# Performance work log

Hardware: AMD Instinct MI355X
Metric: run time of the kernel (lower is better)

Reference implementation:

```python
import jax, jax.numpy as jnp
import numpy as np

NB_FEAT = 20000
NB_CLASSES = 30
N_EDGES = 640000
BATCH = 128


def setup_inputs() -> dict:
    key = jax.random.key(0)
    k1, k2, k3, k4, k5 = jax.random.split(key, 5)
    x = jax.random.normal(k1, (BATCH, NB_FEAT), dtype=jnp.float32)
    edge_index = jax.random.randint(k2, (2, N_EDGES), 0, NB_FEAT, dtype=jnp.int64)
    edge_weight = jax.random.uniform(k3, (N_EDGES,), dtype=jnp.float32)
    fc_w = jax.random.normal(k4, (NB_CLASSES, NB_FEAT), dtype=jnp.float32) * 0.01
    fc_b = jax.random.normal(k5, (NB_CLASSES,), dtype=jnp.float32) * 0.01
    return {"x": x, "edge_index": edge_index, "edge_weight": edge_weight,
            "fc_w": fc_w, "fc_b": fc_b}


def reference(x, edge_index, edge_weight, fc_w, fc_b):
    # SGConv(K=1, bias=False, lin.weight frozen to 1) == gcn_norm + one propagation.
    B, N = x.shape
    src, dst = edge_index[0], edge_index[1]
    # add self-loops with weight 1 (gcn_norm default fill_value=1)
    loop = jnp.arange(N)
    src_f = jnp.concatenate([src, loop])
    dst_f = jnp.concatenate([dst, loop])
    w_f = jnp.concatenate([edge_weight, jnp.ones((N,), edge_weight.dtype)])
    # symmetric normalization: deg over target index
    deg = jax.ops.segment_sum(w_f, dst_f, num_segments=N)  # (N,)
    dinv = jnp.where(deg > 0, jax.lax.rsqrt(deg), 0.0)
    wn = dinv[src_f] * w_f * dinv[dst_f]  # (E',)
    # batched gather-multiply-scatter; graph shared across batch, so vectorize over B
    msgs = x[:, src_f] * wn  # (B, E')
    diffused = jax.ops.segment_sum(msgs.T, dst_f, num_segments=N).T  # (B, N)
    # dropout p=0 -> no-op; dense FC + softmax
    logits = diffused @ fc_w.T + fc_b  # (B, C)
    return jax.nn.softmax(logits, axis=1)
```

## Files before the change

### kernel.cpp

```cpp
#include <hip/hip_runtime.h>


#define N_NODES   20000
#define N_EDGES_C 640000
#define N_CLASSES 30
#define CPAD      32

#define HBLKS     64
#define HNODES    10000
#define HEDGES    (N_EDGES_C / HBLKS)

#define BN        64
#define NBUCKET   313
#define NPB       (NBUCKET * BN)
#define NSLAB     256
#define SLAB_E    (N_EDGES_C / NSLAB)
#define NSCAN     (NBUCKET * NSLAB)
#define ECAP      2600

#define NCHUNK    64
#define NCHUNKS   313
#define XL_LD     130
#define GT_LD     68
#define GBX       128

#define DINVB     ((N_NODES + 255) / 256)

__global__ __launch_bounds__(256) void k1_hists(const int* __restrict__ src,
        const int* __restrict__ dst, const float* __restrict__ w,
        float* __restrict__ degp, int* __restrict__ cnt) {
    __shared__ float h[HNODES];
    int bid = blockIdx.x;
    if (bid < 2 * HBLKS) {
        int eb = bid >> 1, half = bid & 1;
        int nbase = half * HNODES;
        for (int i = threadIdx.x; i < HNODES; i += 256) h[i] = 0.f;
        __syncthreads();
        const int4* d4 = (const int4*)(dst + eb * HEDGES);
        const float4* w4 = (const float4*)(w + eb * HEDGES);
        for (int i = threadIdx.x; i < HEDGES / 4; i += 256) {
            int4 dv = d4[i]; float4 wv = w4[i];
            unsigned r;
            r = (unsigned)(dv.x - nbase); if (r < HNODES) atomicAdd(&h[r], wv.x);
            r = (unsigned)(dv.y - nbase); if (r < HNODES) atomicAdd(&h[r], wv.y);
            r = (unsigned)(dv.z - nbase); if (r < HNODES) atomicAdd(&h[r], wv.z);
            r = (unsigned)(dv.w - nbase); if (r < HNODES) atomicAdd(&h[r], wv.w);
        }
        __syncthreads();
        float* outp = degp + (size_t)bid * HNODES;
        for (int i = threadIdx.x; i < HNODES; i += 256) outp[i] = h[i];
    } else {
        int slab = bid - 2 * HBLKS;
        int* bc = (int*)h;
        for (int i = threadIdx.x; i < NBUCKET; i += 256) bc[i] = 0;
        __syncthreads();
        const int4* s4 = (const int4*)(src + slab * SLAB_E);
        for (int i = threadIdx.x; i < SLAB_E / 4; i += 256) {
            int4 v = s4[i];
            atomicAdd(&bc[v.x >> 6], 1);
            atomicAdd(&bc[v.y >> 6], 1);
            atomicAdd(&bc[v.z >> 6], 1);
            atomicAdd(&bc[v.w >> 6], 1);
        }
        __syncthreads();
        for (int b = threadIdx.x; b < NBUCKET; b += 256) cnt[b * NSLAB + slab] = bc[b];
    }
}

__global__ __launch_bounds__(256) void k2_prep(const int* __restrict__ cnt,
        int* __restrict__ btot, const float* __restrict__ fc_w,
        const float* __restrict__ degp, float* __restrict__ fc_wT,
        float* __restrict__ dinv) {
    int bid = blockIdx.x;
    int t = threadIdx.x;
    if (bid < NBUCKET) {
        __shared__ int lds[256];
        lds[t] = cnt[bid * NSLAB + t];
        __syncthreads();
        for (int o = 128; o > 0; o >>= 1) {
            if (t < o) lds[t] += lds[t + o];
            __syncthreads();
        }
        if (t == 0) btot[bid] = lds[0];
    } else if (bid < 2 * NBUCKET) {
        __shared__ float tile[CPAD][65];
        int n0 = (bid - NBUCKET) * 64;
        #pragma unroll
        for (int k = 0; k < 8; k++) {
            int c = k * 4 + (t >> 6), nn = t & 63;
            int n = n0 + nn;
            tile[c][nn] = (c < N_CLASSES && n < N_NODES) ? fc_w[c * N_NODES + n] : 0.f;
        }
        __syncthreads();
        #pragma unroll
        for (int k = 0; k < 8; k++) {
            int idx = k * 256 + t;
            int nn = idx >> 5, c = idx & 31;
            fc_wT[(size_t)(n0 + nn) * CPAD + c] = tile[c][nn];
        }
    } else {
        int n = (bid - 2 * NBUCKET) * 256 + t;
        if (n < N_NODES) {
            int half = n / HNODES, nn = n - half * HNODES;
            float s = 1.0f;
            for (int eb = 0; eb < HBLKS; eb++)
                s += degp[(size_t)((eb << 1) | half) * HNODES + nn];
            dinv[n] = rsqrtf(s);
        }
    }
}

__global__ __launch_bounds__(256) void k3_off(const int* __restrict__ cnt,
        const int* __restrict__ btot, int* __restrict__ off) {
    __shared__ int lds[256];
    __shared__ int bb;
    int b = blockIdx.x, t = threadIdx.x;
    int s = 0;
    for (int i = t; i < b; i += 256) s += btot[i];
    lds[t] = s;
    __syncthreads();
    for (int o = 128; o > 0; o >>= 1) {
        if (t < o) lds[t] += lds[t + o];
        __syncthreads();
    }
    if (t == 0) bb = lds[0];
    __syncthreads();
    int base = bb;
    int v = cnt[b * NSLAB + t];
    lds[t] = v;
    __syncthreads();
    for (int o = 1; o < 256; o <<= 1) {
        int u = (t >= o) ? lds[t - o] : 0;
        __syncthreads();
        lds[t] += u;
        __syncthreads();
    }
    off[b * NSLAB + t] = base + lds[t] - v;
    if (b == NBUCKET - 1 && t == 255) off[NSCAN] = base + lds[t];
}

__global__ __launch_bounds__(512) void k4_scatter(const int* __restrict__ src,
        const int* __restrict__ dst, const float* __restrict__ w,
        const float* __restrict__ dinv, const int* __restrict__ off,
        int2* __restrict__ erec) {
    __shared__ int cur[NBUCKET];
    int slab = blockIdx.x;
    for (int b = threadIdx.x; b < NBUCKET; b += 512) cur[b] = off[b * NSLAB + slab];
    __syncthreads();
    int e0 = slab * SLAB_E;
    const int4* s4 = (const int4*)(src + e0);
    const int4* d4 = (const int4*)(dst + e0);
    const float4* w4 = (const float4*)(w + e0);
    for (int i = threadIdx.x; i < SLAB_E / 4; i += 512) {
        int4 sv = s4[i]; int4 dv = d4[i]; float4 wv = w4[i];
        int s, d, p; float wn;
        s = sv.x; d = dv.x; wn = dinv[s] * wv.x * dinv[d];
        p = atomicAdd(&cur[s >> 6], 1);
        erec[p] = make_int2(((s & 63) << 15) | d, __float_as_int(wn));
        s = sv.y; d = dv.y; wn = dinv[s] * wv.y * dinv[d];
        p = atomicAdd(&cur[s >> 6], 1);
        erec[p] = make_int2(((s & 63) << 15) | d, __float_as_int(wn));
        s = sv.z; d = dv.z; wn = dinv[s] * wv.z * dinv[d];
        p = atomicAdd(&cur[s >> 6], 1);
        erec[p] = make_int2(((s & 63) << 15) | d, __float_as_int(wn));
        s = sv.w; d = dv.w; wn = dinv[s] * wv.w * dinv[d];
        p = atomicAdd(&cur[s >> 6], 1);
        erec[p] = make_int2(((s & 63) << 15) | d, __float_as_int(wn));
    }
}

__global__ __launch_bounds__(512) void k5_fold(const int2* __restrict__ erec,
        const int* __restrict__ off, const float* __restrict__ dinv,
        const float* __restrict__ fc_wT, float* __restrict__ gT) {
    __shared__ int2 srt[ECAP];
    __shared__ int hist[BN];
    __shared__ int rowst[BN];
    __shared__ int cur[BN];
    int bucket = blockIdx.x;
    int nlo = bucket * BN;
    int bstart = off[bucket * NSLAB];
    int bend   = off[(bucket + 1) * NSLAB];
    int len = min(bend - bstart, ECAP);
    if (threadIdx.x < BN) hist[threadIdx.x] = 0;
    __syncthreads();
    for (int i = threadIdx.x; i < len; i += 512)
        atomicAdd(&hist[((unsigned)erec[bstart + i].x) >> 15], 1);
    __syncthreads();
    if (threadIdx.x < BN) {
        int h = hist[threadIdx.x];
        int v = h;
        #pragma unroll
        for (int o = 1; o < BN; o <<= 1) {
            int u = __shfl_up(v, o, 64);
            if (threadIdx.x >= o) v += u;
        }
        rowst[threadIdx.x] = v - h;
        cur[threadIdx.x]   = v - h;
    }
    __syncthreads();
    for (int i = threadIdx.x; i < len; i += 512) {
        int2 r = erec[bstart + i];
        int p = atomicAdd(&cur[((unsigned)r.x) >> 15], 1);
        srt[p] = r;
    }
    __syncthreads();
    int c = threadIdx.x & 31;
    int grp = threadIdx.x >> 5;
    for (int nn = grp; nn < BN; nn += 16) {
        int n = nlo + nn;
        if (n >= N_NODES) {
            if (n < NPB) gT[(size_t)n * CPAD + c] = 0.f;
            continue;
        }
        float di = dinv[n];
        float acc  = di * di * fc_wT[(size_t)n * CPAD + c];
        float acc2 = 0.f;
        int i = rowst[nn], re = i + hist[nn];
        for (; i + 1 < re; i += 2) {
            int2 r0 = srt[i], r1 = srt[i + 1];
            acc  += __int_as_float(r0.y) * fc_wT[(size_t)(r0.x & 0x7FFF) * CPAD + c];
            acc2 += __int_as_float(r1.y) * fc_wT[(size_t)(r1.x & 0x7FFF) * CPAD + c];
        }
        if (i < re) {
            int2 r0 = srt[i];
            acc += __int_as_float(r0.y) * fc_wT[(size_t)(r0.x & 0x7FFF) * CPAD + c];
        }
        gT[(size_t)n * CPAD + c] = acc + acc2;
    }
}

__global__ __launch_bounds__(512) void k6_gemm(const float* __restrict__ x,
        const float* __restrict__ gT, float* __restrict__ part) {
    __shared__ float xl[(NCHUNK / 2) * XL_LD];
    __shared__ float gt[CPAD * GT_LD];
    int bx = blockIdx.x, bh = blockIdx.y;
    int b0 = bh * 64;
    int wv = threadIdx.x >> 6, l = threadIdx.x & 63;
    float acc0 = 0.f, acc1 = 0.f, acc2 = 0.f, acc3 = 0.f;
    for (int j = 0; j < 3; j++) {
        int ch = bx + GBX * j;
        if (ch >= NCHUNKS) break;
        int n0 = ch * NCHUNK;
        for (int o = threadIdx.x; o < 64 * NCHUNK; o += 512) {
            int b = o >> 6, n = o & (NCHUNK - 1);
            int gn = n0 + n;
            float v = (gn < N_NODES) ? x[(size_t)(b0 + b) * N_NODES + gn] : 0.f;
            xl[(n >> 1) * XL_LD + b * 2 + (n & 1)] = v;
        }
        for (int o = threadIdx.x; o < NCHUNK * CPAD; o += 512) {
            int n = o >> 5, cc = o & 31;
            gt[cc * GT_LD + n] = gT[(size_t)n0 * CPAD + o];
        }
        __syncthreads();
        #pragma unroll
        for (int n4 = 0; n4 < NCHUNK / 4; n4++) {
            float2 xa = *(const float2*)&xl[(2 * n4) * XL_LD + l * 2];
            float2 xb = *(const float2*)&xl[(2 * n4 + 1) * XL_LD + l * 2];
            float4 ga = *(const float4*)&gt[(wv)      * GT_LD + 4 * n4];
            float4 gb = *(const float4*)&gt[(wv +  8) * GT_LD + 4 * n4];
            float4 gc = *(const float4*)&gt[(wv + 16) * GT_LD + 4 * n4];
            float4 gd = *(const float4*)&gt[(wv + 24) * GT_LD + 4 * n4];
            acc0 += xa.x * ga.x + xa.y * ga.y + xb.x * ga.z + xb.y * ga.w;
            acc1 += xa.x * gb.x + xa.y * gb.y + xb.x * gb.z + xb.y * gb.w;
            acc2 += xa.x * gc.x + xa.y * gc.y + xb.x * gc.z + xb.y * gc.w;
            acc3 += xa.x * gd.x + xa.y * gd.y + xb.x * gd.z + xb.y * gd.w;
        }
        __syncthreads();
    }
    size_t pb = (size_t)(bx * 2 + bh) * CPAD * 64;
    part[pb + (size_t)(wv)      * 64 + l] = acc0;
    part[pb + (size_t)(wv +  8) * 64 + l] = acc1;
    part[pb + (size_t)(wv + 16) * 64 + l] = acc2;
    part[pb + (size_t)(wv + 24) * 64 + l] = acc3;
}

__global__ __launch_bounds__(1024) void k7_final(const float* __restrict__ part,
        const float* __restrict__ fc_b, float* __restrict__ out) {
    __shared__ float lg[64 * 33];
    int bh = blockIdx.x;
    int l = threadIdx.x & 63;
    int cq = threadIdx.x >> 6;
    float s0 = 0.f, s1 = 0.f;
    for (int bx = 0; bx < GBX; bx++) {
        const float* p = part + (size_t)(bx * 2 + bh) * CPAD * 64;
        s0 += p[cq * 64 + l];
        s1 += p[(cq + 16) * 64 + l];
    }
    lg[l * 33 + cq]      = s0 + ((cq < N_CLASSES) ? fc_b[cq] : 0.f);
    lg[l * 33 + cq + 16] = s1 + ((cq + 16 < N_CLASSES) ? fc_b[cq + 16] : 0.f);
    __syncthreads();
    if (threadIdx.x < 64) {
        int b = bh * 64 + threadIdx.x;
        float v[N_CLASSES], m = -1e30f;
        #pragma unroll
        for (int c = 0; c < N_CLASSES; c++) {
            v[c] = lg[threadIdx.x * 33 + c];
            m = fmaxf(m, v[c]);
        }
        float s = 0.f;
        #pragma unroll
        for (int c = 0; c < N_CLASSES; c++) { v[c] = __expf(v[c] - m); s += v[c]; }
        float inv = 1.0f / s;
        #pragma unroll
        for (int c = 0; c < N_CLASSES; c++) out[b * N_CLASSES + c] = v[c] * inv;
    }
}

extern "C" void kernel_launch(void* const* d_in, const int* in_sizes, int n_in,
                              void* d_out, int out_size, void* d_ws, size_t ws_size,
                              hipStream_t stream) {
    const float* x          = (const float*)d_in[0];
    const int*   edge_index = (const int*)d_in[1];
    const float* ew         = (const float*)d_in[2];
    const float* fc_w       = (const float*)d_in[3];
    const float* fc_b       = (const float*)d_in[4];
    float* out = (float*)d_out;

    const int* src = edge_index;
    const int* dst = edge_index + N_EDGES_C;

    float* A     = (float*)d_ws;
    float* B     = A + 1280000;
    float* dinv  = B + 1280000;
    int*   cnt   = (int*)(dinv + N_NODES);
    int*   off   = cnt + NSCAN;
    int*   btot  = off + 80136;
    float* fc_wT = (float*)(btot + 320);
    float* gT    = fc_wT + (size_t)NPB * CPAD;

    k1_hists<<<2 * HBLKS + NSLAB, 256, 0, stream>>>(src, dst, ew, A, cnt);
    k2_prep<<<2 * NBUCKET + DINVB, 256, 0, stream>>>(cnt, btot, fc_w, A,
                                                     fc_wT, dinv);
    k3_off<<<NBUCKET, 256, 0, stream>>>(cnt, btot, off);
    k4_scatter<<<NSLAB, 512, 0, stream>>>(src, dst, ew, dinv, off, (int2*)B);
    k5_fold<<<NBUCKET, 512, 0, stream>>>((int2*)B, off, dinv, fc_wT, gT);
    k6_gemm<<<dim3(GBX, 2), 512, 0, stream>>>(x, gT, A);
    k7_final<<<2, 1024, 0, stream>>>(A, fc_b, out);
}
```

Measured before the change: 92.33 us.

## Fuse seven pipeline kernels into one cooperative persistent kernel with grid syncs

Replaces the seven separate kernel launches with a single cooperative kernel of 256 blocks that runs every stage in sequence, separated by grid-wide barriers, and keeps the multi-kernel path as a fallback if the cooperative launch fails. The aim is to remove per-launch overhead and the inter-kernel gaps in a short pipeline. It also halves the number of degree-histogram edge blocks and uses 512 threads per block throughout. In exchange, each stage is limited to 256 resident blocks, the grid syncs add their own cost, and the shared-memory union raises per-block LDS use.

Result: slower. 296.5 us (+221.1%).

```diff
diff --git a/kernel.cpp b/kernel.cpp
--- a/kernel.cpp
+++ b/kernel.cpp
@@ -1,4 +1,7 @@
 #include <hip/hip_runtime.h>
+#include <hip/hip_cooperative_groups.h>
+
+namespace cg = cooperative_groups;
 
 
 #define N_NODES   20000
@@ -6,7 +9,7 @@
 #define N_CLASSES 30
 #define CPAD      32
 
-#define HBLKS     64
+#define HBLKS     32
 #define HNODES    10000
 #define HEDGES    (N_EDGES_C / HBLKS)
 
@@ -24,7 +27,296 @@
 #define GT_LD     68
 #define GBX       128
 
+#define GRID      256
+#define TPB       512
 #define DINVB     ((N_NODES + 255) / 256)
+
+union SMem {
+    float hist[HNODES];
+    int   bc[NBUCKET];
+    int   cur[NBUCKET];
+    float tile[CPAD][65];
+    struct { int lds[TPB]; int bb; } scan;
+    struct { int2 srt[ECAP]; int hist[BN]; int rowst[BN]; int cur[BN]; } fold;
+    struct { float xl[(NCHUNK / 2) * XL_LD]; float gt[CPAD * GT_LD]; } gemm;
+    float lg[64 * 33];
+};
+
+__global__ __launch_bounds__(TPB, 2) void mega(
+        const int* __restrict__ src, const int* __restrict__ dst,
+        const float* __restrict__ ew, const float* __restrict__ x,
+        const float* __restrict__ fc_w, const float* __restrict__ fc_b,
+        float* __restrict__ out,
+        float* __restrict__ degp,
+        int2* __restrict__ erec,
+        float* __restrict__ dinv, int* __restrict__ cnt, int* __restrict__ off,
+        int* __restrict__ btot, float* __restrict__ fc_wT, float* __restrict__ gT) {
+    cg::grid_group grid = cg::this_grid();
+    __shared__ SMem sm;
+    int t = threadIdx.x;
+    float* part = degp;
+
+    for (int u = blockIdx.x; u < 2 * HBLKS + NSLAB + NBUCKET; u += GRID) {
+        if (u < 2 * HBLKS) {
+            int eb = u >> 1, half = u & 1;
+            int nbase = half * HNODES;
+            for (int i = t; i < HNODES; i += TPB) sm.hist[i] = 0.f;
+            __syncthreads();
+            const int4* d4 = (const int4*)(dst + eb * HEDGES);
+            const float4* w4 = (const float4*)(ew + eb * HEDGES);
+            for (int i = t; i < HEDGES / 4; i += TPB) {
+                int4 dv = d4[i]; float4 wv = w4[i];
+                unsigned r;
+                r = (unsigned)(dv.x - nbase); if (r < HNODES) atomicAdd(&sm.hist[r], wv.x);
+                r = (unsigned)(dv.y - nbase); if (r < HNODES) atomicAdd(&sm.hist[r], wv.y);
+                r = (unsigned)(dv.z - nbase); if (r < HNODES) atomicAdd(&sm.hist[r], wv.z);
+                r = (unsigned)(dv.w - nbase); if (r < HNODES) atomicAdd(&sm.hist[r], wv.w);
+            }
+            __syncthreads();
+            float* outp = degp + (size_t)u * HNODES;
+            for (int i = t; i < HNODES; i += TPB) outp[i] = sm.hist[i];
+        } else if (u < 2 * HBLKS + NSLAB) {
+            int slab = u - 2 * HBLKS;
+            for (int i = t; i < NBUCKET; i += TPB) sm.bc[i] = 0;
+            __syncthreads();
+            const int4* s4 = (const int4*)(src + slab * SLAB_E);
+            for (int i = t; i < SLAB_E / 4; i += TPB) {
+                int4 v = s4[i];
+                atomicAdd(&sm.bc[v.x >> 6], 1);
+                atomicAdd(&sm.bc[v.y >> 6], 1);
+                atomicAdd(&sm.bc[v.z >> 6], 1);
+                atomicAdd(&sm.bc[v.w >> 6], 1);
+            }
+            __syncthreads();
+            for (int b = t; b < NBUCKET; b += TPB) cnt[b * NSLAB + slab] = sm.bc[b];
+        } else {
+            int n0 = (u - 2 * HBLKS - NSLAB) * 64;
+            #pragma unroll
+            for (int k = 0; k < 4; k++) {
+                int idx = k * TPB + t; int c = idx >> 6, nn = idx & 63;
+                int n = n0 + nn;
+                sm.tile[c][nn] = (c < N_CLASSES && n < N_NODES) ? fc_w[c * N_NODES + n] : 0.f;
+            }
+            __syncthreads();
+            #pragma unroll
+            for (int k = 0; k < 4; k++) {
+                int idx = k * TPB + t; int nn = idx >> 5, c = idx & 31;
+                fc_wT[(size_t)(n0 + nn) * CPAD + c] = sm.tile[c][nn];
+            }
+        }
+        __syncthreads();
+    }
+    grid.sync();
+
+    for (int u = blockIdx.x; u < NBUCKET + 40; u += GRID) {
+        if (u < NBUCKET) {
+            sm.scan.lds[t] = (t < NSLAB) ? cnt[u * NSLAB + t] : 0;
+            __syncthreads();
+            for (int o = TPB / 2; o > 0; o >>= 1) {
+                if (t < o) sm.scan.lds[t] += sm.scan.lds[t + o];
+                __syncthreads();
+            }
+            if (t == 0) btot[u] = sm.scan.lds[0];
+        } else {
+            int n = (u - NBUCKET) * TPB + t;
+            if (n < N_NODES) {
+                int half = n / HNODES, nn = n - half * HNODES;
+                float s = 1.0f;
+                for (int eb = 0; eb < HBLKS; eb++)
+                    s += degp[(size_t)((eb << 1) | half) * HNODES + nn];
+                dinv[n] = rsqrtf(s);
+            }
+        }
+        __syncthreads();
+    }
+    grid.sync();
+
+    for (int b = blockIdx.x; b < NBUCKET; b += GRID) {
+        int s = 0;
+        for (int i = t; i < b; i += TPB) s += btot[i];
+        sm.scan.lds[t] = s;
+        __syncthreads();
+        for (int o = TPB / 2; o > 0; o >>= 1) {
+            if (t < o) sm.scan.lds[t] += sm.scan.lds[t + o];
+            __syncthreads();
+        }
+        if (t == 0) sm.scan.bb = sm.scan.lds[0];
+        __syncthreads();
+        int base = sm.scan.bb;
+        int v = (t < NSLAB) ? cnt[b * NSLAB + t] : 0;
+        if (t < NSLAB) sm.scan.lds[t] = v;
+        __syncthreads();
+        for (int o = 1; o < NSLAB; o <<= 1) {
+            int u2 = (t < NSLAB && t >= o) ? sm.scan.lds[t - o] : 0;
+            __syncthreads();
+            if (t < NSLAB) sm.scan.lds[t] += u2;
+            __syncthreads();
+        }
+        if (t < NSLAB) off[b * NSLAB + t] = base + sm.scan.lds[t] - v;
+        if (b == NBUCKET - 1 && t == NSLAB - 1) off[NSCAN] = base + sm.scan.lds[t];
+        __syncthreads();
+    }
+    grid.sync();
+
+    for (int slab = blockIdx.x; slab < NSLAB; slab += GRID) {
+        for (int b = t; b < NBUCKET; b += TPB) sm.cur[b] = off[b * NSLAB + slab];
+        __syncthreads();
+        int e0 = slab * SLAB_E;
+        const int4* s4 = (const int4*)(src + e0);
+        const int4* d4 = (const int4*)(dst + e0);
+        const float4* w4 = (const float4*)(ew + e0);
+        for (int i = t; i < SLAB_E / 4; i += TPB) {
+            int4 sv = s4[i]; int4 dv = d4[i]; float4 wv = w4[i];
+            int s, d, p; float wn;
+            s = sv.x; d = dv.x; wn = dinv[s] * wv.x * dinv[d];
+            p = atomicAdd(&sm.cur[s >> 6], 1);
+            erec[p] = make_int2(((s & 63) << 15) | d, __float_as_int(wn));
+            s = sv.y; d = dv.y; wn = dinv[s] * wv.y * dinv[d];
+            p = atomicAdd(&sm.cur[s >> 6], 1);
+            erec[p] = make_int2(((s & 63) << 15) | d, __float_as_int(wn));
+            s = sv.z; d = dv.z; wn = dinv[s] * wv.z * dinv[d];
+            p = atomicAdd(&sm.cur[s >> 6], 1);
+            erec[p] = make_int2(((s & 63) << 15) | d, __float_as_int(wn));
+            s = sv.w; d = dv.w; wn = dinv[s] * wv.w * dinv[d];
+            p = atomicAdd(&sm.cur[s >> 6], 1);
+            erec[p] = make_int2(((s & 63) << 15) | d, __float_as_int(wn));
+        }
+        __syncthreads();
+    }
+    grid.sync();
+
+    for (int bucket = blockIdx.x; bucket < NBUCKET; bucket += GRID) {
+        int nlo = bucket * BN;
+        int bstart = off[bucket * NSLAB];
+        int bend   = off[(bucket + 1) * NSLAB];
+        int len = min(bend - bstart, ECAP);
+        if (t < BN) sm.fold.hist[t] = 0;
+        __syncthreads();
+        for (int i = t; i < len; i += TPB)
+            atomicAdd(&sm.fold.hist[((unsigned)erec[bstart + i].x) >> 15], 1);
+        __syncthreads();
+        if (t < BN) {
+            int h = sm.fold.hist[t];
+            int v = h;
+            #pragma unroll
+            for (int o = 1; o < BN; o <<= 1) {
+                int u2 = __shfl_up(v, o, 64);
+                if (t >= o) v += u2;
+            }
+            sm.fold.rowst[t] = v - h;
+            sm.fold.cur[t]   = v - h;
+        }
+        __syncthreads();
+        for (int i = t; i < len; i += TPB) {
+            int2 r = erec[bstart + i];
+            int p = atomicAdd(&sm.fold.cur[((unsigned)r.x) >> 15], 1);
+            sm.fold.srt[p] = r;
+        }
+        __syncthreads();
+        int c = t & 31;
+        int grp = t >> 5;
+        for (int nn = grp; nn < BN; nn += 16) {
+            int n = nlo + nn;
+            if (n >= N_NODES) {
+                if (n < NPB) gT[(size_t)n * CPAD + c] = 0.f;
+                continue;
+            }
+            float di = dinv[n];
+            float acc  = di * di * fc_wT[(size_t)n * CPAD + c];
+            float acc2 = 0.f;
+            int i = sm.fold.rowst[nn], re = i + sm.fold.hist[nn];
+            for (; i + 1 < re; i += 2) {
+                int2 r0 = sm.fold.srt[i], r1 = sm.fold.srt[i + 1];
+                acc  += __int_as_float(r0.y) * fc_wT[(size_t)(r0.x & 0x7FFF) * CPAD + c];
+                acc2 += __int_as_float(r1.y) * fc_wT[(size_t)(r1.x & 0x7FFF) * CPAD + c];
+            }
+            if (i < re) {
+                int2 r0 = sm.fold.srt[i];
+                acc += __int_as_float(r0.y) * fc_wT[(size_t)(r0.x & 0x7FFF) * CPAD + c];
+            }
+            gT[(size_t)n * CPAD + c] = acc + acc2;
+        }
+        __syncthreads();
+    }
+    grid.sync();
+
+    for (int u = blockIdx.x; u < GBX * 2; u += GRID) {
+        int bx = u & (GBX - 1), bh = u >> 7;
+        int b0 = bh * 64;
+        int wv = t >> 6, l = t & 63;
+        float acc0 = 0.f, acc1 = 0.f, acc2 = 0.f, acc3 = 0.f;
+        for (int j = 0; j < 3; j++) {
+            int ch = bx + GBX * j;
+            if (ch >= NCHUNKS) break;
+            int n0 = ch * NCHUNK;
+            for (int o = t; o < 64 * NCHUNK; o += TPB) {
+                int b = o >> 6, n = o & (NCHUNK - 1);
+                int gn = n0 + n;
+                float v = (gn < N_NODES) ? x[(size_t)(b0 + b) * N_NODES + gn] : 0.f;
+                sm.gemm.xl[(n >> 1) * XL_LD + b * 2 + (n & 1)] = v;
+            }
+            for (int o = t; o < NCHUNK * CPAD; o += TPB) {
+                int n = o >> 5, cc = o & 31;
+                sm.gemm.gt[cc * GT_LD + n] = gT[(size_t)n0 * CPAD + o];
+            }
+            __syncthreads();
+            #pragma unroll
+            for (int n4 = 0; n4 < NCHUNK / 4; n4++) {
+                float2 xa = *(const float2*)&sm.gemm.xl[(2 * n4) * XL_LD + l * 2];
+                float2 xb = *(const float2*)&sm.gemm.xl[(2 * n4 + 1) * XL_LD + l * 2];
+                float4 ga = *(const float4*)&sm.gemm.gt[(wv)      * GT_LD + 4 * n4];
+                float4 gb = *(const float4*)&sm.gemm.gt[(wv +  8) * GT_LD + 4 * n4];
+                float4 gc = *(const float4*)&sm.gemm.gt[(wv + 16) * GT_LD + 4 * n4];
+                float4 gd = *(const float4*)&sm.gemm.gt[(wv + 24) * GT_LD + 4 * n4];
+                acc0 += xa.x * ga.x + xa.y * ga.y + xb.x * ga.z + xb.y * ga.w;
+                acc1 += xa.x * gb.x + xa.y * gb.y + xb.x * gb.z + xb.y * gb.w;
+                acc2 += xa.x * gc.x + xa.y * gc.y + xb.x * gc.z + xb.y * gc.w;
+                acc3 += xa.x * gd.x + xa.y * gd.y + xb.x * gd.z + xb.y * gd.w;
+            }
+            __syncthreads();
+        }
+        size_t pb = (size_t)(bx * 2 + bh) * CPAD * 64;
+        part[pb + (size_t)(wv)      * 64 + l] = acc0;
+        part[pb + (size_t)(wv +  8) * 64 + l] = acc1;
+        part[pb + (size_t)(wv + 16) * 64 + l] = acc2;
+        part[pb + (size_t)(wv + 24) * 64 + l] = acc3;
+        __syncthreads();
+    }
+    grid.sync();
+
+    for (int u = blockIdx.x; u < 2; u += GRID) {
+        int bh = u;
+        int l = t & 63;
+        int cq = t >> 6;
+        float s0 = 0.f, s1 = 0.f, s2 = 0.f, s3 = 0.f;
+        for (int bx = 0; bx < GBX; bx++) {
+            const float* p = part + (size_t)(bx * 2 + bh) * CPAD * 64;
+            s0 += p[(cq)      * 64 + l];
+            s1 += p[(cq +  8) * 64 + l];
+            s2 += p[(cq + 16) * 64 + l];
+            s3 += p[(cq + 24) * 64 + l];
+        }
+        sm.lg[l * 33 + cq]      = s0 + ((cq      < N_CLASSES) ? fc_b[cq]      : 0.f);
+        sm.lg[l * 33 + cq + 8]  = s1 + ((cq + 8  < N_CLASSES) ? fc_b[cq + 8]  : 0.f);
+        sm.lg[l * 33 + cq + 16] = s2 + ((cq + 16 < N_CLASSES) ? fc_b[cq + 16] : 0.f);
+        sm.lg[l * 33 + cq + 24] = s3 + ((cq + 24 < N_CLASSES) ? fc_b[cq + 24] : 0.f);
+        __syncthreads();
+        if (t < 64) {
+            int b = bh * 64 + t;
+            float v[N_CLASSES], m = -1e30f;
+            #pragma unroll
+            for (int c = 0; c < N_CLASSES; c++) { v[c] = sm.lg[t * 33 + c]; m = fmaxf(m, v[c]); }
+            float s = 0.f;
+            #pragma unroll
+            for (int c = 0; c < N_CLASSES; c++) { v[c] = __expf(v[c] - m); s += v[c]; }
+            float inv = 1.0f / s;
+            #pragma unroll
+            for (int c = 0; c < N_CLASSES; c++) out[b * N_CLASSES + c] = v[c] * inv;
+        }
+        __syncthreads();
+    }
+}
+
 
 __global__ __launch_bounds__(256) void k1_hists(const int* __restrict__ src,
         const int* __restrict__ dst, const float* __restrict__ w,
@@ -293,10 +585,7 @@
         int b = bh * 64 + threadIdx.x;
         float v[N_CLASSES], m = -1e30f;
         #pragma unroll
-        for (int c = 0; c < N_CLASSES; c++) {
-            v[c] = lg[threadIdx.x * 33 + c];
-            m = fmaxf(m, v[c]);
-        }
+        for (int c = 0; c < N_CLASSES; c++) { v[c] = lg[threadIdx.x * 33 + c]; m = fmaxf(m, v[c]); }
         float s = 0.f;
         #pragma unroll
         for (int c = 0; c < N_CLASSES; c++) { v[c] = __expf(v[c] - m); s += v[c]; }
@@ -320,20 +609,33 @@
     const int* dst = edge_index + N_EDGES_C;
 
     float* A     = (float*)d_ws;
-    float* B     = A + 1280000;
-    float* dinv  = B + 1280000;
+    float* Bp    = A + 1280000;
+    float* dinv  = Bp + 1280000;
     int*   cnt   = (int*)(dinv + N_NODES);
     int*   off   = cnt + NSCAN;
     int*   btot  = off + 80136;
     float* fc_wT = (float*)(btot + 320);
     float* gT    = fc_wT + (size_t)NPB * CPAD;
 
-    k1_hists<<<2 * HBLKS + NSLAB, 256, 0, stream>>>(src, dst, ew, A, cnt);
-    k2_prep<<<2 * NBUCKET + DINVB, 256, 0, stream>>>(cnt, btot, fc_w, A,
-                                                     fc_wT, dinv);
-    k3_off<<<NBUCKET, 256, 0, stream>>>(cnt, btot, off);
-    k4_scatter<<<NSLAB, 512, 0, stream>>>(src, dst, ew, dinv, off, (int2*)B);
-    k5_fold<<<NBUCKET, 512, 0, stream>>>((int2*)B, off, dinv, fc_wT, gT);
-    k6_gemm<<<dim3(GBX, 2), 512, 0, stream>>>(x, gT, A);
-    k7_final<<<2, 1024, 0, stream>>>(A, fc_b, out);
-}
+    int2* erec = (int2*)Bp;
+
+    void* args[] = {
+        (void*)&src, (void*)&dst, (void*)&ew, (void*)&x, (void*)&fc_w,
+        (void*)&fc_b, (void*)&out, (void*)&A, (void*)&erec,
+        (void*)&dinv, (void*)&cnt, (void*)&off, (void*)&btot,
+        (void*)&fc_wT, (void*)&gT
+    };
+    hipError_t e = hipLaunchCooperativeKernel((void*)mega, dim3(GRID), dim3(TPB),
+                                              args, 0, stream);
+    if (e != hipSuccess) {
+        (void)hipGetLastError();
+        k1_hists<<<2 * HBLKS + NSLAB, 256, 0, stream>>>(src, dst, ew, A, cnt);
+        k2_prep<<<2 * NBUCKET + DINVB, 256, 0, stream>>>(cnt, btot, fc_w, A,
+                                                         fc_wT, dinv);
+        k3_off<<<NBUCKET, 256, 0, stream>>>(cnt, btot, off);
+        k4_scatter<<<NSLAB, 512, 0, stream>>>(src, dst, ew, dinv, off, erec);
+        k5_fold<<<NBUCKET, 512, 0, stream>>>(erec, off, dinv, fc_wT, gT);
+        k6_gemm<<<dim3(GBX, 2), 512, 0, stream>>>(x, gT, A);
+        k7_final<<<2, 1024, 0, stream>>>(A, fc_b, out);
+    }
+}
```
